# Performance work log

Hardware: AMD Instinct MI355X
Metric: run time of the kernel (lower is better)

The kernel has to match this reference:

```python
import jax, jax.numpy as jnp
import numpy as np
import math

NUM_HEADS = 8
KEY_DIM = 32
VALUE_DIM = 32
ERF = 3                      # local window (erf x erf), N = 1 + ERF*ERF key/query positions
PAD = (ERF - 1) // 2
STRIDE = 2
OUT_CH = 256


def unfold_2d(x, k, p, s):
    """Mirror of F.unfold -> (B, k*k, C, Ho, Wo), window index row-major (kh, kw)."""
    B, C, H, W = x.shape
    xp = jnp.pad(x, ((0, 0), (0, 0), (p, p), (p, p)))
    Ho = (H + 2 * p - k) // s + 1
    Wo = (W + 2 * p - k) // s + 1
    pats = [xp[:, :, i:i + s * (Ho - 1) + 1:s, j:j + s * (Wo - 1) + 1:s]
            for i in range(k) for j in range(k)]
    return jnp.stack(pats, axis=1)


def fold_2d(pats, out_hw, k, p, s):
    """Mirror of F.fold (overlap-add inverse of unfold_2d)."""
    B, kk, C, Ho, Wo = pats.shape
    H, W = out_hw
    out = jnp.zeros((B, C, H + 2 * p, W + 2 * p), pats.dtype)
    idx = 0
    for i in range(k):
        for j in range(k):
            out = out.at[:, :, i:i + s * (Ho - 1) + 1:s, j:j + s * (Wo - 1) + 1:s].add(pats[:, idx])
            idx += 1
    return out[:, :, p:p + H, p:p + W]


def setup_inputs() -> dict:
    key = jax.random.key(0)
    ks = jax.random.split(key, 10)
    B = 2
    d = {
        "top_feat": jax.random.normal(ks[0], (B, OUT_CH, 64, 64), jnp.float32),
        "bot_feat": jax.random.normal(ks[1], (B, OUT_CH, 128, 128), jnp.float32),
    }
    qkv_names = ["W_top_key", "W_top_query", "W_top_value", "W_bot_key", "W_bot_query", "W_bot_value"]
    for n, kk in zip(qkv_names, ks[2:8]):
        out_dim = NUM_HEADS * (KEY_DIM if ("key" in n or "query" in n) else VALUE_DIM)
        d[n] = 0.01 * jax.random.normal(kk, (out_dim, OUT_CH), jnp.float32)  # 1x1 conv, no bias
    d["W_top_fuse"] = 0.01 * jax.random.normal(ks[8], (OUT_CH, NUM_HEADS * VALUE_DIM), jnp.float32)
    d["W_bot_fuse"] = 0.01 * jax.random.normal(ks[9], (OUT_CH, NUM_HEADS * VALUE_DIM), jnp.float32)
    return d


def _forward(top_feat, bot_feat, W_top_key, W_top_query, W_top_value,
             W_bot_key, W_bot_query, W_bot_value, W_top_fuse, W_bot_fuse):
    B, _, H, W = top_feat.shape
    Hb, Wb = bot_feat.shape[2], bot_feat.shape[3]

    def proj(x, Wm, dim):  # 1x1 conv then split heads -> (B, h, dim, H', W')
        y = jnp.einsum('oc,bchw->bohw', Wm, x)
        return y.reshape(B, NUM_HEADS, dim, x.shape[2], x.shape[3])

    def unfold_heads(x):  # (B, h, d, Hb, Wb) -> (B, h, e*e, d, H, W)
        d = x.shape[2]
        u = unfold_2d(x.reshape(B * NUM_HEADS, d, Hb, Wb), ERF, PAD, STRIDE)
        return u.reshape(B, NUM_HEADS, ERF * ERF, d, u.shape[3], u.shape[4])

    tK = proj(top_feat, W_top_key, KEY_DIM)[:, :, None]      # (B, h, 1, kd, H, W)
    tQ = proj(top_feat, W_top_query, KEY_DIM)[:, :, None]
    tV = proj(top_feat, W_top_value, VALUE_DIM)[:, :, None]
    bK = unfold_heads(proj(bot_feat, W_bot_key, KEY_DIM))    # (B, h, e*e, kd, H, W)
    bQ = unfold_heads(proj(bot_feat, W_bot_query, KEY_DIM))
    bV = unfold_heads(proj(bot_feat, W_bot_value, VALUE_DIM))

    key_ = jnp.concatenate([tK, bK], axis=2)   # (B, h, N, kd, H, W), N = 1 + e*e
    query = jnp.concatenate([tQ, bQ], axis=2)
    value = jnp.concatenate([tV, bV], axis=2)

    # weight[b,n,k,q,h,w] = <key_k, query_q> / sqrt(kd)   (NOTE: no softmax in original)
    weight = jnp.einsum('bnkdhw,bnqdhw->bnkqhw', key_, query) / math.sqrt(KEY_DIM)
    # out[b,n,q,v,h,w] = sum_k weight[...] * value_k
    out = jnp.einsum('bnkqhw,bnkvhw->bnqvhw', weight, value)  # (B, h, N, vd, H, W)

    top_ret = out[:, :, 0].reshape(B, NUM_HEADS * VALUE_DIM, H, W)
    bot_pat = out[:, :, 1:].reshape(B * NUM_HEADS, ERF * ERF, VALUE_DIM, H, W)
    bot_ret = fold_2d(bot_pat, (Hb, Wb), ERF, PAD, STRIDE).reshape(B, NUM_HEADS * VALUE_DIM, Hb, Wb)

    top_out = jnp.einsum('oc,bchw->bohw', W_top_fuse, top_ret)
    bot_out = jnp.einsum('oc,bchw->bohw', W_bot_fuse, bot_ret)
    return top_out, bot_out


def reference(top_feat, bot_feat, W_top_key, W_top_query, W_top_value,
              W_bot_key, W_bot_query, W_bot_value, W_top_fuse, W_bot_fuse):
    return _forward(top_feat, bot_feat, W_top_key, W_top_query, W_top_value,
                    W_bot_key, W_bot_query, W_bot_value, W_top_fuse, W_bot_fuse)
```

## Files before the change

kernel.cpp:

```cpp
#include <hip/hip_runtime.h>
#include <hip/hip_bf16.h>
#include <math.h>


typedef __attribute__((ext_vector_type(8))) short  bh8;
typedef __attribute__((ext_vector_type(4))) short  bh4;
typedef __attribute__((ext_vector_type(4))) float  f32x4;
typedef unsigned short u16;

static __device__ __forceinline__ u16 f2b(float x) {
    __hip_bfloat16 h = __float2bfloat16(x);
    return __builtin_bit_cast(u16, h);
}
static __device__ __forceinline__ float b2f(u16 u) {
    unsigned v = ((unsigned)u) << 16;
    return __builtin_bit_cast(float, v);
}

static __device__ __forceinline__ void gload16(const u16* g, u16* l) {
    __builtin_amdgcn_global_load_lds(
        (const __attribute__((address_space(1))) unsigned int*)g,
        (__attribute__((address_space(3))) unsigned int*)l, 16, 0, 0);
}

__global__ __launch_bounds__(256) void k_cvt_w(
    const float* w0, const float* w1, const float* w2, const float* w3,
    const float* w4, const float* w5, const float* w6, const float* w7,
    u16* __restrict__ Wb)
{
    const float* srcs[8] = {w0,w1,w2,w3,w4,w5,w6,w7};
    const float* src = srcs[blockIdx.y];
    int i = (blockIdx.x * 256 + threadIdx.x) * 4;
    float4 v = *(const float4*)&src[i];
    u16 tmp[4] = { f2b(v.x), f2b(v.y), f2b(v.z), f2b(v.w) };
    *(uint2*)&Wb[(size_t)blockIdx.y * 65536 + i] = *(uint2*)tmp;
}

__global__ __launch_bounds__(256) void k_proj(
    const float* __restrict__ top_feat, const float* __restrict__ bot_feat,
    const u16* __restrict__ Wb,
    u16* __restrict__ tK, u16* __restrict__ bK, size_t TOPU, size_t BOTU)
{
    const int yb    = blockIdx.y;
    const bool istop = yb < 128;
    const float* feat = istop ? top_feat : bot_feat;
    const u16* Bw   = istop ? Wb : (Wb + 3 * 65536);
    u16* Yp         = istop ? tK : bK;
    const size_t arrsz = istop ? TOPU : BOTU;
    const int S     = istop ? 4096 : 16384;
    const int m0g   = (istop ? yb : (yb - 128)) * 64;
    const int b     = istop ? (m0g >> 12) : (m0g >> 14);
    const int pix0  = m0g & (S - 1);
    const float* Xb = feat + (size_t)b * 256 * S;
    const int n0 = blockIdx.x * 256;
    const int t  = threadIdx.x;
    const int w  = t >> 6, wl = t & 63, l16 = wl & 15, grp = wl >> 4;
    const int apix = t & 63;
    const int aq   = t >> 6;

    __shared__ __align__(16) u16 AT[2][64 * 64];
    __shared__ __align__(16) u16 BT[2][256 * 64];

    float rA[2][8];

#define PROJ_A_LOAD(kk) do {                                                  \
        _Pragma("unroll")                                                     \
        for (int cc = 0; cc < 2; ++cc)                                        \
            _Pragma("unroll")                                                 \
            for (int e = 0; e < 8; ++e)                                       \
                rA[cc][e] = Xb[(size_t)((kk) + (2*aq + cc)*8 + e) * S         \
                               + pix0 + apix];                                \
    } while (0)

#define PROJ_A_WRITE(bufi) do {                                               \
        _Pragma("unroll")                                                     \
        for (int cc = 0; cc < 2; ++cc) {                                      \
            int cg = 2*aq + cc, slot = cg ^ (apix & 7);                       \
            u16 tmp[8];                                                       \
            _Pragma("unroll")                                                 \
            for (int e = 0; e < 8; ++e) tmp[e] = f2b(rA[cc][e]);              \
            *(uint4*)&AT[bufi][apix * 64 + slot * 8] = *(uint4*)tmp;          \
        }                                                                     \
    } while (0)

#define PROJ_STAGE_B(bufi, kk) do {                                           \
        _Pragma("unroll")                                                     \
        for (int it = 0; it < 8; ++it) {                                      \
            int lin = it * 256 + t;                                           \
            int row = lin >> 3, c = lin & 7;                                  \
            int cs = c ^ (row & 7);                                           \
            gload16(&Bw[(size_t)(n0 + row) * 256 + (kk) + cs * 8],            \
                    &BT[bufi][lin * 8]);                                      \
        }                                                                     \
    } while (0)

    f32x4 acc[4][4];
    #pragma unroll
    for (int i = 0; i < 4; ++i)
        #pragma unroll
        for (int j = 0; j < 4; ++j) acc[i][j] = (f32x4){0.f, 0.f, 0.f, 0.f};

    PROJ_A_LOAD(0);
    PROJ_STAGE_B(0, 0);
    PROJ_A_WRITE(0);
    int cur = 0;
    for (int kt = 0; kt < 4; ++kt) {
        __syncthreads();
        if (kt < 3) {
            PROJ_A_LOAD((kt + 1) * 64);
            PROJ_STAGE_B(cur ^ 1, (kt + 1) * 64);
        }
        #pragma unroll
        for (int ks = 0; ks < 2; ++ks) {
            bh8 af[4], bf[4];
            #pragma unroll
            for (int mi = 0; mi < 4; ++mi) {
                int row = mi * 16 + l16;
                int pc = (ks * 4 + grp) ^ (row & 7);
                af[mi] = *(const bh8*)&AT[cur][row * 64 + pc * 8];
            }
            #pragma unroll
            for (int ni = 0; ni < 4; ++ni) {
                int row = w * 64 + ni * 16 + l16;
                int pc = (ks * 4 + grp) ^ (row & 7);
                bf[ni] = *(const bh8*)&BT[cur][row * 64 + pc * 8];
            }
            #pragma unroll
            for (int mi = 0; mi < 4; ++mi)
                #pragma unroll
                for (int ni = 0; ni < 4; ++ni)
                    acc[mi][ni] = __builtin_amdgcn_mfma_f32_16x16x32_bf16(
                        af[mi], bf[ni], acc[mi][ni], 0, 0, 0);
        }
        if (kt < 3) PROJ_A_WRITE(cur ^ 1);
        cur ^= 1;
    }
#undef PROJ_A_LOAD
#undef PROJ_A_WRITE
#undef PROJ_STAGE_B

    #pragma unroll
    for (int mi = 0; mi < 4; ++mi)
        #pragma unroll
        for (int ni = 0; ni < 4; ++ni)
            #pragma unroll
            for (int r = 0; r < 4; ++r) {
                int m = m0g + mi*16 + grp*4 + r;
                int n = n0 + w*64 + ni*16 + l16;
                Yp[(size_t)(n >> 8) * arrsz + (size_t)m * 256 + (n & 255)]
                    = f2b(acc[mi][ni][r]);
            }
}

#define GEMM_STAGE(bufi, kk) do {                                             \
        _Pragma("unroll")                                                     \
        for (int it = 0; it < 2; ++it) {                                      \
            int lin = it * 256 + t;                                           \
            int row = lin >> 3, c = lin & 7;                                  \
            int cs = c ^ (row & 7);                                           \
            gload16(&A[(size_t)(m0 + row) * 256 + (kk) + cs * 8],             \
                    &AT[bufi][lin * 8]);                                      \
        }                                                                     \
        _Pragma("unroll")                                                     \
        for (int it = 0; it < 8; ++it) {                                      \
            int lin = it * 256 + t;                                           \
            int row = lin >> 3, c = lin & 7;                                  \
            int cs = c ^ (row & 7);                                           \
            gload16(&B[(size_t)(n0 + row) * 256 + (kk) + cs * 8],             \
                    &BT[bufi][lin * 8]);                                      \
        }                                                                     \
    } while (0)

#define GEMM_MAIN()                                                           \
    GEMM_STAGE(0, 0);                                                         \
    int cur = 0;                                                              \
    for (int kt = 0; kt < 4; ++kt) {                                          \
        __syncthreads();                                                      \
        if (kt < 3) GEMM_STAGE(cur ^ 1, (kt + 1) * 64);                       \
        _Pragma("unroll")                                                     \
        for (int ks = 0; ks < 2; ++ks) {                                      \
            bh8 af[4], bf[4];                                                 \
            _Pragma("unroll")                                                 \
            for (int mi = 0; mi < 4; ++mi) {                                  \
                int row = mi * 16 + l16;                                      \
                int pc = (ks * 4 + grp) ^ (row & 7);                          \
                af[mi] = *(const bh8*)&AT[cur][row * 64 + pc * 8];            \
            }                                                                 \
            _Pragma("unroll")                                                 \
            for (int ni = 0; ni < 4; ++ni) {                                  \
                int row = w * 64 + ni * 16 + l16;                             \
                int pc = (ks * 4 + grp) ^ (row & 7);                          \
                bf[ni] = *(const bh8*)&BT[cur][row * 64 + pc * 8];            \
            }                                                                 \
            _Pragma("unroll")                                                 \
            for (int mi = 0; mi < 4; ++mi)                                    \
                _Pragma("unroll")                                             \
                for (int ni = 0; ni < 4; ++ni)                                \
                    acc[mi][ni] = __builtin_amdgcn_mfma_f32_16x16x32_bf16(    \
                        af[mi], bf[ni], acc[mi][ni], 0, 0, 0);                \
        }                                                                     \
        cur ^= 1;                                                             \
    }

__global__ __launch_bounds__(256) void k_fuse(
    const u16* __restrict__ Wb, const u16* __restrict__ tRet,
    const u16* __restrict__ botRet, float* __restrict__ top_out,
    float* __restrict__ bot_out)
{
    const int bid = blockIdx.x;
    const u16* A; const u16* B; float* Yf; int lgS, n0, m0;
    if (bid < 128) {
        A = Wb + 6 * 65536; B = tRet; Yf = top_out; lgS = 12;
        n0 = (bid & 31) * 256; m0 = (bid >> 5) * 64;
    } else {
        int i = bid - 128;
        A = Wb + 7 * 65536; B = botRet; Yf = bot_out; lgS = 14;
        n0 = (i & 127) * 256; m0 = (i >> 7) * 64;
    }
    const int t  = threadIdx.x;
    const int w  = t >> 6, wl = t & 63, l16 = wl & 15, grp = wl >> 4;

    __shared__ __align__(16) u16 AT[2][64 * 64];
    __shared__ __align__(16) u16 BT[2][256 * 64];

    f32x4 acc[4][4];
    #pragma unroll
    for (int i = 0; i < 4; ++i)
        #pragma unroll
        for (int j = 0; j < 4; ++j) acc[i][j] = (f32x4){0.f, 0.f, 0.f, 0.f};

    GEMM_MAIN();

    #pragma unroll
    for (int mi = 0; mi < 4; ++mi)
        #pragma unroll
        for (int ni = 0; ni < 4; ++ni)
            #pragma unroll
            for (int r = 0; r < 4; ++r) {
                int m = m0 + mi*16 + grp*4 + r;
                int n = n0 + w*64 + ni*16 + l16;
                int bb = n >> lgS, s = n & ((1 << lgS) - 1);
                Yf[(((size_t)bb * 256 + m) << lgS) + s] = acc[mi][ni][r];
            }
}

__global__ __launch_bounds__(256) void k_attn(
    const u16* __restrict__ tK, const u16* __restrict__ tQ, const u16* __restrict__ tV,
    const u16* __restrict__ bK, const u16* __restrict__ bQ, const u16* __restrict__ bV,
    u16* __restrict__ tRet, u16* __restrict__ pat)
{
    const int pix = blockIdx.x;
    const int b   = blockIdx.y;
    const int w   = threadIdx.x >> 6;
    const int wl  = threadIdx.x & 63;
    const int l16 = wl & 15, grp = wl >> 4;
    const int y = pix >> 6, x = pix & 63;

    __shared__ u16 Ssm[4][16][24];
    __shared__ __align__(16) u16 Vsm[4][2][16][16];

    const int p = l16;
    bool pvalid = false; int bpix = 0; const bool istop = (p == 0);
    if (p == 0) pvalid = true;
    else if (p < 10) {
        int pm = p - 1; int i = (pm * 11) >> 5; int j = pm - 3 * i;
        int by = 2 * y + i - 1, bx = 2 * x + j - 1;
        pvalid = ((unsigned)by < 128u) && ((unsigned)bx < 128u);
        bpix = by * 128 + bx;
    }
    const size_t topRow = ((size_t)b * 4096  + pix)  * 256;
    const size_t botRow = ((size_t)b * 16384 + bpix) * 256;
    const float scale = 0.17677669529663687f;

    #pragma unroll
    for (int hi = 0; hi < 2; ++hi) {
        const int h = w + hi * 4;
        const size_t off = (istop ? topRow : botRow) + h * 32 + grp * 8;
        bh8 aQ = {}, aK = {}, vV = {};
        if (pvalid) {
            if (istop) {
                aQ = *(const bh8*)(tQ + off);
                aK = *(const bh8*)(tK + off);
                vV = *(const bh8*)(tV + off);
            } else {
                aQ = *(const bh8*)(bQ + off);
                aK = *(const bh8*)(bK + off);
                vV = *(const bh8*)(bV + off);
            }
        }
        *(bh8*)&Vsm[w][grp >> 1][p][(grp & 1) * 8] = vV;

        f32x4 z = {0.f, 0.f, 0.f, 0.f};
        f32x4 sC = __builtin_amdgcn_mfma_f32_16x16x32_bf16(aQ, aK, z, 0, 0, 0);
        #pragma unroll
        for (int r = 0; r < 4; ++r)
            Ssm[w][grp * 4 + r][l16] = f2b(sC[r] * scale);

        bh8 aS = {};
        *(bh4*)&aS = *(const bh4*)&Ssm[w][l16][grp * 4];

        bh8 bv0 = {}, bv1 = {};
        #pragma unroll
        for (int j = 0; j < 4; ++j) {
            bv0[j] = (short)Vsm[w][0][grp * 4 + j][l16];
            bv1[j] = (short)Vsm[w][1][grp * 4 + j][l16];
        }
        f32x4 oc0 = __builtin_amdgcn_mfma_f32_16x16x32_bf16(aS, bv0, z, 0, 0, 0);
        f32x4 oc1 = __builtin_amdgcn_mfma_f32_16x16x32_bf16(aS, bv1, z, 0, 0, 0);

        if (grp == 0) {
            size_t o = topRow + (size_t)h * 32;
            tRet[o + l16]      = f2b(oc0[0]);
            tRet[o + 16 + l16] = f2b(oc1[0]);
        }
        #pragma unroll
        for (int r = 0; r < 4; ++r) {
            int q = grp * 4 + r;
            if (q >= 1 && q <= 9) {
                size_t base = ((((size_t)b * 8 + h) * 9 + (q - 1)) * 4096 + pix) * 32;
                pat[base + l16]      = f2b(oc0[r]);
                pat[base + 16 + l16] = f2b(oc1[r]);
            }
        }
    }
}

__global__ __launch_bounds__(256) void k_fold(
    const u16* __restrict__ pat, u16* __restrict__ botRet)
{
    int tid = blockIdx.x * 256 + threadIdx.x;
    int vchunk = tid & 3;
    int ri = tid >> 2;
    int b = ri >> 17;
    int bpix = (ri >> 3) & 16383;
    int h = ri & 7;
    int by = bpix >> 7, bx = bpix & 127;
    int v0 = vchunk * 8;

    float acc[8];
    #pragma unroll
    for (int e = 0; e < 8; ++e) acc[e] = 0.f;

    for (int iy = 0; iy < 3; ++iy) {
        int ty = by + 1 - iy;
        if (ty & 1) continue;
        int yy = ty >> 1;
        if ((unsigned)yy >= 64u) continue;
        for (int jx = 0; jx < 3; ++jx) {
            int tx = bx + 1 - jx;
            if (tx & 1) continue;
            int xx = tx >> 1;
            if ((unsigned)xx >= 64u) continue;
            int q = iy * 3 + jx;
            size_t addr = ((((size_t)b * 8 + h) * 9 + q) * 4096 + (yy * 64 + xx)) * 32 + v0;
            uint4 pv = *(const uint4*)&pat[addr];
            const u16* pp = (const u16*)&pv;
            #pragma unroll
            for (int e = 0; e < 8; ++e) acc[e] += b2f(pp[e]);
        }
    }
    u16 tmp[8];
    #pragma unroll
    for (int e = 0; e < 8; ++e) tmp[e] = f2b(acc[e]);
    *(uint4*)&botRet[((size_t)b * 16384 + bpix) * 256 + h * 32 + v0] = *(uint4*)tmp;
}

extern "C" void kernel_launch(void* const* d_in, const int* in_sizes, int n_in,
                              void* d_out, int out_size, void* d_ws, size_t ws_size,
                              hipStream_t stream) {
    const float* top_feat = (const float*)d_in[0];
    const float* bot_feat = (const float*)d_in[1];

    float* out     = (float*)d_out;
    float* top_out = out;
    float* bot_out = out + (size_t)2 * 256 * 4096;

    const size_t TOPU = (size_t)2 * 4096  * 256;
    const size_t BOTU = (size_t)2 * 16384 * 256;
    char* p = (char*)d_ws;
    u16* Wb     = (u16*)p;  p += (size_t)8 * 65536 * 2;
    u16* tK     = (u16*)p;  p += TOPU * 2;
    u16* tQ     = (u16*)p;  p += TOPU * 2;
    u16* tV     = (u16*)p;  p += TOPU * 2;
    u16* bK     = (u16*)p;  p += BOTU * 2;
    u16* bQ     = (u16*)p;  p += BOTU * 2;
    u16* bV     = (u16*)p;  p += BOTU * 2;
    u16* tRet   = (u16*)p;  p += TOPU * 2;
    u16* pat    = (u16*)p;  p += (size_t)2*8*9*4096*32*2;
    u16* botRet = (u16*)p;  p += BOTU * 2;

    dim3 blk(256);

    k_cvt_w<<<dim3(64, 8), blk, 0, stream>>>(
        (const float*)d_in[2], (const float*)d_in[3], (const float*)d_in[4],
        (const float*)d_in[5], (const float*)d_in[6], (const float*)d_in[7],
        (const float*)d_in[8], (const float*)d_in[9], Wb);

    k_proj<<<dim3(3, 640), blk, 0, stream>>>(top_feat, bot_feat, Wb,
                                             tK, bK, TOPU, BOTU);

    k_attn<<<dim3(4096, 2), blk, 0, stream>>>(tK, tQ, tV, bK, bQ, bV, tRet, pat);

    k_fold<<<dim3(4096), blk, 0, stream>>>(pat, botRet);

    k_fuse<<<dim3(640), blk, 0, stream>>>(Wb, tRet, botRet, top_out, bot_out);
}
```

Baseline: 102.3 us.

## Deepen projection GEMM pipeline with K=32 tiles and register-staged B prefetch

The QKV projection kernel now uses K-tiles of 32 instead of 64, halving shared memory per stage, and keeps two tiles of prefetched global data in registers, so global loads run two iterations ahead of compute. Weight tiles are staged through registers instead of direct global-to-LDS loads, with a new XOR swizzle for the 32-wide rows. This is meant to hide global load latency better and possibly raise occupancy through lower LDS use, at the cost of more registers, twice as many barriers, and extra VGPR-to-LDS store instructions.

After: 172.5 us. 68.6% more time.

```diff
diff --git a/kernel.cpp b/kernel.cpp
--- a/kernel.cpp
+++ b/kernel.cpp
@@ -58,39 +58,43 @@
     const int apix = t & 63;
     const int aq   = t >> 6;
 
-    __shared__ __align__(16) u16 AT[2][64 * 64];
-    __shared__ __align__(16) u16 BT[2][256 * 64];
+    __shared__ __align__(16) u16 AT[2][64 * 32];
+    __shared__ __align__(16) u16 BT[2][256 * 32];
 
     float rA[2][8];
-
-#define PROJ_A_LOAD(kk) do {                                                  \
-        _Pragma("unroll")                                                     \
-        for (int cc = 0; cc < 2; ++cc)                                        \
-            _Pragma("unroll")                                                 \
-            for (int e = 0; e < 8; ++e)                                       \
-                rA[cc][e] = Xb[(size_t)((kk) + (2*aq + cc)*8 + e) * S         \
-                               + pix0 + apix];                                \
+    uint4 rB[2][4];
+
+#define PA_LOAD(set, kk) do {                                                 \
+        _Pragma("unroll")                                                     \
+        for (int e = 0; e < 8; ++e)                                           \
+            rA[set][e] = Xb[(size_t)((kk) + aq * 8 + e) * S + pix0 + apix];   \
     } while (0)
 
-#define PROJ_A_WRITE(bufi) do {                                               \
-        _Pragma("unroll")                                                     \
-        for (int cc = 0; cc < 2; ++cc) {                                      \
-            int cg = 2*aq + cc, slot = cg ^ (apix & 7);                       \
-            u16 tmp[8];                                                       \
-            _Pragma("unroll")                                                 \
-            for (int e = 0; e < 8; ++e) tmp[e] = f2b(rA[cc][e]);              \
-            *(uint4*)&AT[bufi][apix * 64 + slot * 8] = *(uint4*)tmp;          \
+#define PA_WRITE(bufi, set) do {                                              \
+        u16 tmp[8];                                                           \
+        _Pragma("unroll")                                                     \
+        for (int e = 0; e < 8; ++e) tmp[e] = f2b(rA[set][e]);                 \
+        int slot = aq ^ ((apix >> 1) & 3);                                    \
+        *(uint4*)&AT[bufi][apix * 32 + slot * 8] = *(uint4*)tmp;              \
+    } while (0)
+
+#define PB_LOAD(set, kk) do {                                                 \
+        _Pragma("unroll")                                                     \
+        for (int it = 0; it < 4; ++it) {                                      \
+            int lin = it * 256 + t;                                           \
+            int row = lin >> 2, c = lin & 3;                                  \
+            rB[set][it] = *(const uint4*)&Bw[(size_t)(n0 + row) * 256         \
+                                             + (kk) + c * 8];                 \
         }                                                                     \
     } while (0)
 
-#define PROJ_STAGE_B(bufi, kk) do {                                           \
-        _Pragma("unroll")                                                     \
-        for (int it = 0; it < 8; ++it) {                                      \
+#define PB_WRITE(bufi, set) do {                                              \
+        _Pragma("unroll")                                                     \
+        for (int it = 0; it < 4; ++it) {                                      \
             int lin = it * 256 + t;                                           \
-            int row = lin >> 3, c = lin & 7;                                  \
-            int cs = c ^ (row & 7);                                           \
-            gload16(&Bw[(size_t)(n0 + row) * 256 + (kk) + cs * 8],            \
-                    &BT[bufi][lin * 8]);                                      \
+            int row = lin >> 2, c = lin & 3;                                  \
+            int slot = c ^ ((row >> 1) & 3);                                  \
+            *(uint4*)&BT[bufi][row * 32 + slot * 8] = rB[set][it];            \
         }                                                                     \
     } while (0)
 
@@ -100,44 +104,46 @@
         #pragma unroll
         for (int j = 0; j < 4; ++j) acc[i][j] = (f32x4){0.f, 0.f, 0.f, 0.f};
 
-    PROJ_A_LOAD(0);
-    PROJ_STAGE_B(0, 0);
-    PROJ_A_WRITE(0);
-    int cur = 0;
-    for (int kt = 0; kt < 4; ++kt) {
+    PA_LOAD(0, 0);  PA_LOAD(1, 32);
+    PB_LOAD(0, 0);  PB_LOAD(1, 32);
+    PA_WRITE(0, 0); PB_WRITE(0, 0);
+
+    #pragma unroll
+    for (int kt = 0; kt < 8; ++kt) {
+        const int cur = kt & 1;
         __syncthreads();
-        if (kt < 3) {
-            PROJ_A_LOAD((kt + 1) * 64);
-            PROJ_STAGE_B(cur ^ 1, (kt + 1) * 64);
-        }
-        #pragma unroll
-        for (int ks = 0; ks < 2; ++ks) {
-            bh8 af[4], bf[4];
+        if (kt < 6) {
+            PA_LOAD(cur, (kt + 2) * 32);
+            PB_LOAD(cur, (kt + 2) * 32);
+        }
+        bh8 af[4], bf[4];
+        #pragma unroll
+        for (int mi = 0; mi < 4; ++mi) {
+            int row = mi * 16 + l16;
+            int slot = grp ^ ((row >> 1) & 3);
+            af[mi] = *(const bh8*)&AT[cur][row * 32 + slot * 8];
+        }
+        #pragma unroll
+        for (int ni = 0; ni < 4; ++ni) {
+            int row = w * 64 + ni * 16 + l16;
+            int slot = grp ^ ((row >> 1) & 3);
+            bf[ni] = *(const bh8*)&BT[cur][row * 32 + slot * 8];
+        }
+        #pragma unroll
+        for (int mi = 0; mi < 4; ++mi)
             #pragma unroll
-            for (int mi = 0; mi < 4; ++mi) {
-                int row = mi * 16 + l16;
-                int pc = (ks * 4 + grp) ^ (row & 7);
-                af[mi] = *(const bh8*)&AT[cur][row * 64 + pc * 8];
-            }
-            #pragma unroll
-            for (int ni = 0; ni < 4; ++ni) {
-                int row = w * 64 + ni * 16 + l16;
-                int pc = (ks * 4 + grp) ^ (row & 7);
-                bf[ni] = *(const bh8*)&BT[cur][row * 64 + pc * 8];
-            }
-            #pragma unroll
-            for (int mi = 0; mi < 4; ++mi)
-                #pragma unroll
-                for (int ni = 0; ni < 4; ++ni)
-                    acc[mi][ni] = __builtin_amdgcn_mfma_f32_16x16x32_bf16(
-                        af[mi], bf[ni], acc[mi][ni], 0, 0, 0);
-        }
-        if (kt < 3) PROJ_A_WRITE(cur ^ 1);
-        cur ^= 1;
-    }
-#undef PROJ_A_LOAD
-#undef PROJ_A_WRITE
-#undef PROJ_STAGE_B
+            for (int ni = 0; ni < 4; ++ni)
+                acc[mi][ni] = __builtin_amdgcn_mfma_f32_16x16x32_bf16(
+                    af[mi], bf[ni], acc[mi][ni], 0, 0, 0);
+        if (kt < 7) {
+            PA_WRITE(cur ^ 1, (kt + 1) & 1);
+            PB_WRITE(cur ^ 1, (kt + 1) & 1);
+        }
+    }
+#undef PA_LOAD
+#undef PA_WRITE
+#undef PB_LOAD
+#undef PB_WRITE
 
     #pragma unroll
     for (int mi = 0; mi < 4; ++mi)
```
